# Kernel optimization log

Hardware: AMD Instinct MI355X
Metric: run time of the kernel (lower is better)

Reference implementation:

```python
import jax, jax.numpy as jnp
import numpy as np


def a_powers(A, t):
    # A: [K, n, n]; returns [t, K, n, n] = stack(I, A, A^2, ..., A^(t-1))
    K, n, _ = A.shape
    result = jnp.broadcast_to(jnp.eye(n, dtype=A.dtype), (1, K, n, n))
    lift = A
    while result.shape[0] < t:
        result = jnp.concatenate([result, result @ lift], axis=0)
        lift = lift @ lift
    return result[:t]


def fast_conv_real(a, b):
    # a: [len1, K, n, n], b: [batch, len2, K, n] -> conv(b, a): [batch, len1+len2-1, K, n]
    len1 = a.shape[0]
    len2 = b.shape[1]
    T = 2 ** int(np.ceil(np.log2(len1 + len2 - 1)))
    Af = jnp.fft.rfft(a, n=T, axis=0)
    Bf = jnp.fft.rfft(b, n=T, axis=1)
    Cf = jnp.einsum('blki,lkij->blkj', Bf, Af)
    c = jnp.fft.irfft(Cf, n=T, axis=1)
    return c[:, :len1 + len2 - 1]


def setup_inputs() -> dict:
    key = jax.random.key(0)
    k_u, k_x0, k_theta, k_B, k_C = jax.random.split(key, 5)
    batch, length = 8, 4096
    input_size, state_size, output_size = 256, 256, 256
    blk = 2
    K = state_size // blk  # 128
    u = jax.random.normal(k_u, (batch, length, input_size), dtype=jnp.float32)
    x0 = jax.random.normal(k_x0, (batch, K, blk), dtype=jnp.float32)
    # A initialized as K random 2x2 rotation blocks (as in __init__)
    theta = 2 * jnp.pi * jax.random.uniform(k_theta, (K,), dtype=jnp.float32)
    c, s = jnp.cos(theta), jnp.sin(theta)
    A = jnp.stack([jnp.stack([c, s], -1), jnp.stack([-s, c], -1)], -2)  # [K, 2, 2]
    B = jax.random.normal(k_B, (input_size, state_size), dtype=jnp.float32) / (state_size + input_size) ** 0.5
    C = jax.random.normal(k_C, (state_size, output_size), dtype=jnp.float32) / (state_size + output_size) ** 0.5
    return {"u": u, "x0": x0, "A": A, "B": B, "C": C}


def reference(u, x0, A, B, C):
    batch, length, _ = u.shape
    K, blk, _ = A.shape
    Aps = a_powers(A, length + 1)          # [length+1, K, blk, blk]
    uB = (u @ B).reshape(batch, length, K, blk)
    x = fast_conv_real(Aps[:-1], uB)[:, :length]  # [batch, length, K, blk]
    x = x + jnp.einsum('bki,lkij->blkj', x0, Aps[1:])
    new_state = x[:, -1]                    # [batch, K, blk]
    y = x.reshape(batch, length, K * blk) @ C
    return (y, new_state)
```

## Files before the change

kernel.cpp:

```cpp
#include <hip/hip_runtime.h>
#include <hip/hip_bf16.h>

typedef __bf16 bf16x2_t __attribute__((ext_vector_type(2)));
typedef __bf16 bf16x8_t __attribute__((ext_vector_type(8)));
typedef float f32x4 __attribute__((ext_vector_type(4)));

#define BATCH   8
#define LENGTH  4096
#define KHALF   128
#define MTOT    (BATCH*LENGTH)
#define NCHUNK  128
#define LC      32

#define SWZ(ch, row) ((ch) ^ ((row) & 7))

__global__ __launch_bounds__(256) void transpose_bc(
    const float* __restrict__ Bsrc, const float* __restrict__ Csrc,
    __bf16* __restrict__ BT, __bf16* __restrict__ CT) {
  const float* src = blockIdx.y ? Csrc : Bsrc;
  __bf16* dst      = blockIdx.y ? CT   : BT;
  int n  = blockIdx.x;
  int kk = threadIdx.x;
  dst[n * 256 + kk] = (__bf16)src[kk * 256 + n];
}

__global__ __launch_bounds__(256) void gemm1_fused(
    const float* __restrict__ u, const __bf16* __restrict__ BT,
    const float* __restrict__ Aarr,
    __bf16* __restrict__ uB, float2* __restrict__ P) {
  __shared__ __align__(16) __bf16 sA[64 * 256];

  const int tid  = threadIdx.x;
  const int lane = tid & 63;
  const int wave = tid >> 6;
  const int m_l  = lane & 15, quad = lane >> 4;
  const int m0   = blockIdx.x * 64;
  const int b    = m0 >> 12;
  const int t0   = m0 & 4095;

#pragma unroll
  for (int i = 0; i < 8; ++i) {
    int s   = tid + i * 256;
    int row = s >> 5, ch = s & 31;
    const float4* g = (const float4*)(u + (size_t)(m0 + row) * 256 + ch * 8);
    float4 a = g[0], c = g[1];
    bf16x8_t v;
    v[0]=(__bf16)a.x; v[1]=(__bf16)a.y; v[2]=(__bf16)a.z; v[3]=(__bf16)a.w;
    v[4]=(__bf16)c.x; v[5]=(__bf16)c.y; v[6]=(__bf16)c.z; v[7]=(__bf16)c.w;
    *(bf16x8_t*)&sA[row * 256 + SWZ(ch, row) * 8] = v;
  }
  __syncthreads();

  f32x4 acc[4][4];
#pragma unroll
  for (int mi = 0; mi < 4; ++mi)
#pragma unroll
    for (int ni = 0; ni < 4; ++ni)
#pragma unroll
      for (int r = 0; r < 4; ++r) acc[mi][ni][r] = 0.f;

#pragma unroll
  for (int kc8 = 0; kc8 < 8; ++kc8) {
    bf16x8_t af[4], bfr[4];
#pragma unroll
    for (int mi = 0; mi < 4; ++mi) {
      int row = mi * 16 + m_l;
      int c   = kc8 * 4 + quad;
      af[mi] = *(const bf16x8_t*)&sA[row * 256 + SWZ(c, row) * 8];
    }
#pragma unroll
    for (int ni = 0; ni < 4; ++ni) {
      int n = wave * 64 + ni * 16 + m_l;
      bfr[ni] = *(const bf16x8_t*)(BT + (size_t)n * 256 + kc8 * 32 + quad * 8);
    }
#pragma unroll
    for (int mi = 0; mi < 4; ++mi)
#pragma unroll
      for (int ni = 0; ni < 4; ++ni)
        acc[mi][ni] = __builtin_amdgcn_mfma_f32_16x16x32_bf16(af[mi], bfr[ni], acc[mi][ni], 0, 0, 0);
  }
  __syncthreads();

  __bf16* sT = sA;
#pragma unroll
  for (int mi = 0; mi < 4; ++mi)
#pragma unroll
    for (int ni = 0; ni < 4; ++ni)
#pragma unroll
      for (int r = 0; r < 4; ++r) {
        int row = mi * 16 + quad * 4 + r;
        int col = wave * 64 + ni * 16 + m_l;
        sT[row * 256 + SWZ(col >> 3, row) * 8 + (col & 7)] = (__bf16)acc[mi][ni][r];
      }
  __syncthreads();

#pragma unroll
  for (int i = 0; i < 8; ++i) {
    int s   = tid + i * 256;
    int row = s >> 5, ch = s & 31;
    *(bf16x8_t*)(uB + (size_t)(m0 + row) * 256 + ch * 8) =
        *(const bf16x8_t*)&sT[row * 256 + SWZ(ch, row) * 8];
  }

  {
    int k   = tid & 127;
    int chl = tid >> 7;
    float cc = Aarr[4 * k], sv = Aarr[4 * k + 1];
    float hr = 0.f, hi = 0.f;
#pragma unroll 8
    for (int j = 0; j < LC; ++j) {
      int row = chl * 32 + j;
      bf16x2_t v2 = *(const bf16x2_t*)&sT[row * 256 + SWZ(k >> 2, row) * 8 + ((2 * k) & 7)];
      float t = fmaf(hr, cc, fmaf(-hi, sv, (float)v2[0]));
      hi      = fmaf(hr, sv, fmaf( hi, cc, (float)v2[1]));
      hr = t;
    }
    int chg = (t0 >> 5) + chl;
    P[((size_t)b * NCHUNK + chg) * KHALF + k] = make_float2(hr, hi);
  }
}

__global__ __launch_bounds__(256) void scan_carry2(
    const float* __restrict__ Aarr, const float* __restrict__ x0,
    const float2* __restrict__ P, float2* __restrict__ H,
    float* __restrict__ state_out) {
  const int lane = threadIdx.x & 63;
  const int wv   = threadIdx.x >> 6;
  const int p    = blockIdx.x * 4 + wv;
  const int b    = p >> 7, k = p & 127;
  const float cc = Aarr[4 * k], sv = Aarr[4 * k + 1];

  float wr = cc, wi = sv;
#pragma unroll
  for (int i = 0; i < 5; ++i) { float nr = wr*wr - wi*wi; wi = 2.f*wr*wi; wr = nr; }
  float Wr[6], Wi[6];
  Wr[0] = wr*wr - wi*wi; Wi[0] = 2.f*wr*wi;
#pragma unroll
  for (int s = 1; s < 6; ++s) { Wr[s] = Wr[s-1]*Wr[s-1] - Wi[s-1]*Wi[s-1]; Wi[s] = 2.f*Wr[s-1]*Wi[s-1]; }

  float2 P0 = P[((size_t)b * NCHUNK + 2 * lane)     * KHALF + k];
  float2 P1 = P[((size_t)b * NCHUNK + 2 * lane + 1) * KHALF + k];
  float qr = fmaf(wr, P0.x, fmaf(-wi, P0.y, P1.x));
  float qi = fmaf(wr, P0.y, fmaf( wi, P0.x, P1.y));
  float Sr = qr, Si = qi;
#pragma unroll
  for (int s = 0; s < 6; ++s) {
    float tr = __shfl_up(Sr, 1 << s, 64);
    float ti = __shfl_up(Si, 1 << s, 64);
    if (lane >= (1 << s)) {
      float nSr = fmaf(Wr[s], tr, fmaf(-Wi[s], ti, Sr));
      float nSi = fmaf(Wr[s], ti, fmaf( Wi[s], tr, Si));
      Sr = nSr; Si = nSi;
    }
  }
  float Ar = __shfl_up(Sr, 1, 64), Ai = __shfl_up(Si, 1, 64);
  if (lane == 0) { Ar = 0.f; Ai = 0.f; }
  float pr = 1.f, pi = 0.f;
#pragma unroll
  for (int s = 0; s < 6; ++s)
    if ((lane >> s) & 1) { float nr = pr*Wr[s] - pi*Wi[s]; pi = pr*Wi[s] + pi*Wr[s]; pr = nr; }

  float x0r = x0[b * 256 + 2 * k], x0i = x0[b * 256 + 2 * k + 1];
  float H0r = fmaf(pr, x0r, fmaf(-pi, x0i, Ar));
  float H0i = fmaf(pr, x0i, fmaf( pi, x0r, Ai));
  H[((size_t)b * NCHUNK + 2 * lane) * KHALF + k] = make_float2(H0r, H0i);
  float H1r = fmaf(wr, H0r, fmaf(-wi, H0i, P0.x));
  float H1i = fmaf(wr, H0i, fmaf( wi, H0r, P0.y));
  H[((size_t)b * NCHUNK + 2 * lane + 1) * KHALF + k] = make_float2(H1r, H1i);
  if (lane == 63) {
    state_out[b * 256 + 2 * k]     = fmaf(wr, H1r, fmaf(-wi, H1i, P1.x));
    state_out[b * 256 + 2 * k + 1] = fmaf(wr, H1i, fmaf( wi, H1r, P1.y));
  }
}

__global__ __launch_bounds__(256) void gemm2_fused(
    const __bf16* __restrict__ uB, const float* __restrict__ Aarr,
    const float2* __restrict__ H, const __bf16* __restrict__ CT,
    float* __restrict__ Y) {
  __shared__ __align__(16) __bf16 sX[64 * 256];

  const int tid  = threadIdx.x;
  const int lane = tid & 63;
  const int wave = tid >> 6;
  const int m_l  = lane & 15, quad = lane >> 4;
  const int m0   = blockIdx.x * 64;
  const int b    = m0 >> 12;
  const int t0   = m0 & 4095;

#pragma unroll
  for (int i = 0; i < 8; ++i) {
    int s   = tid + i * 256;
    int row = s >> 5, ch = s & 31;
    *(bf16x8_t*)&sX[row * 256 + SWZ(ch, row) * 8] =
        *(const bf16x8_t*)(uB + (size_t)(m0 + row) * 256 + ch * 8);
  }
  __syncthreads();

  {
    int k   = tid & 127;
    int chl = tid >> 7;
    float cc = Aarr[4 * k], sv = Aarr[4 * k + 1];
    float2 h = H[((size_t)b * NCHUNK + (t0 >> 5) + chl) * KHALF + k];
    float hr = h.x, hi = h.y;
#pragma unroll 8
    for (int j = 0; j < LC; ++j) {
      int row = chl * 32 + j;
      int idx = row * 256 + SWZ(k >> 2, row) * 8 + ((2 * k) & 7);
      bf16x2_t v2 = *(const bf16x2_t*)&sX[idx];
      float t = fmaf(hr, cc, fmaf(-hi, sv, (float)v2[0]));
      hi      = fmaf(hr, sv, fmaf( hi, cc, (float)v2[1]));
      hr = t;
      bf16x2_t o; o[0] = (__bf16)hr; o[1] = (__bf16)hi;
      *(bf16x2_t*)&sX[idx] = o;
    }
  }
  __syncthreads();

  f32x4 acc[4][4];
#pragma unroll
  for (int mi = 0; mi < 4; ++mi)
#pragma unroll
    for (int ni = 0; ni < 4; ++ni)
#pragma unroll
      for (int r = 0; r < 4; ++r) acc[mi][ni][r] = 0.f;

#pragma unroll
  for (int kc8 = 0; kc8 < 8; ++kc8) {
    bf16x8_t af[4], bfr[4];
#pragma unroll
    for (int mi = 0; mi < 4; ++mi) {
      int row = mi * 16 + m_l;
      int c   = kc8 * 4 + quad;
      af[mi] = *(const bf16x8_t*)&sX[row * 256 + SWZ(c, row) * 8];
    }
#pragma unroll
    for (int ni = 0; ni < 4; ++ni) {
      int n = wave * 64 + ni * 16 + m_l;
      bfr[ni] = *(const bf16x8_t*)(CT + (size_t)n * 256 + kc8 * 32 + quad * 8);
    }
#pragma unroll
    for (int mi = 0; mi < 4; ++mi)
#pragma unroll
      for (int ni = 0; ni < 4; ++ni)
        acc[mi][ni] = __builtin_amdgcn_mfma_f32_16x16x32_bf16(af[mi], bfr[ni], acc[mi][ni], 0, 0, 0);
  }

#pragma unroll
  for (int mi = 0; mi < 4; ++mi)
#pragma unroll
    for (int ni = 0; ni < 4; ++ni)
#pragma unroll
      for (int r = 0; r < 4; ++r) {
        int row = m0 + mi * 16 + quad * 4 + r;
        int col = wave * 64 + ni * 16 + m_l;
        Y[(size_t)row * 256 + col] = acc[mi][ni][r];
      }
}

extern "C" void kernel_launch(void* const* d_in, const int* in_sizes, int n_in,
                              void* d_out, int out_size, void* d_ws, size_t ws_size,
                              hipStream_t stream) {
  const float* u  = (const float*)d_in[0];
  const float* x0 = (const float*)d_in[1];
  const float* A  = (const float*)d_in[2];
  const float* B  = (const float*)d_in[3];
  const float* C  = (const float*)d_in[4];

  float* y         = (float*)d_out;
  float* state_out = y + (size_t)MTOT * 256;

  char* ws = (char*)d_ws;
  __bf16* BT = (__bf16*)ws;  ws += 256 * 256 * 2;
  __bf16* CT = (__bf16*)ws;  ws += 256 * 256 * 2;
  __bf16* uB = (__bf16*)ws;  ws += (size_t)MTOT * 256 * 2;
  float2* P  = (float2*)ws;  ws += (size_t)BATCH * NCHUNK * KHALF * sizeof(float2);
  float2* H  = (float2*)ws;  ws += (size_t)BATCH * NCHUNK * KHALF * sizeof(float2);

  transpose_bc<<<dim3(256, 2), 256, 0, stream>>>(B, C, BT, CT);
  gemm1_fused<<<dim3(MTOT / 64), 256, 0, stream>>>(u, BT, A, uB, P);
  scan_carry2<<<dim3(256), 256, 0, stream>>>(A, x0, P, H, state_out);
  gemm2_fused<<<dim3(MTOT / 64), 256, 0, stream>>>(uB, A, H, CT, y);
}
```

Before: 119.4 us.

## Recompute u@B in output kernel instead of storing uB; fold carry scan inline

The first kernel no longer writes the bf16 uB intermediate and only emits per-chunk partial states P. The output kernel rereads u, recomputes the u@B GEMM, and computes each chunk's incoming carry by serially combining the preceding chunk partials from x0. This drops the separate scan kernel and one launch. It also removes the 16MB uB write and read. The cost is a second GEMM over u, a serial loop of up to 127 steps per thread, and a 32MB fp32 reread of u.

```diff
diff --git a/kernel.cpp b/kernel.cpp
--- a/kernel.cpp
+++ b/kernel.cpp
@@ -24,11 +24,10 @@
   dst[n * 256 + kk] = (__bf16)src[kk * 256 + n];
 }
 
-__global__ __launch_bounds__(256) void gemm1_fused(
+__global__ __launch_bounds__(256, 2) void gemm_p(
     const float* __restrict__ u, const __bf16* __restrict__ BT,
-    const float* __restrict__ Aarr,
-    __bf16* __restrict__ uB, float2* __restrict__ P) {
-  __shared__ __align__(16) __bf16 sA[64 * 256];
+    const float* __restrict__ Aarr, float2* __restrict__ P) {
+  __shared__ __align__(16) __bf16 sT[64 * 256];
 
   const int tid  = threadIdx.x;
   const int lane = tid & 63;
@@ -47,7 +46,7 @@
     bf16x8_t v;
     v[0]=(__bf16)a.x; v[1]=(__bf16)a.y; v[2]=(__bf16)a.z; v[3]=(__bf16)a.w;
     v[4]=(__bf16)c.x; v[5]=(__bf16)c.y; v[6]=(__bf16)c.z; v[7]=(__bf16)c.w;
-    *(bf16x8_t*)&sA[row * 256 + SWZ(ch, row) * 8] = v;
+    *(bf16x8_t*)&sT[row * 256 + SWZ(ch, row) * 8] = v;
   }
   __syncthreads();
 
@@ -66,7 +65,7 @@
     for (int mi = 0; mi < 4; ++mi) {
       int row = mi * 16 + m_l;
       int c   = kc8 * 4 + quad;
-      af[mi] = *(const bf16x8_t*)&sA[row * 256 + SWZ(c, row) * 8];
+      af[mi] = *(const bf16x8_t*)&sT[row * 256 + SWZ(c, row) * 8];
     }
 #pragma unroll
     for (int ni = 0; ni < 4; ++ni) {
@@ -81,7 +80,6 @@
   }
   __syncthreads();
 
-  __bf16* sT = sA;
 #pragma unroll
   for (int mi = 0; mi < 4; ++mi)
 #pragma unroll
@@ -93,14 +91,6 @@
         sT[row * 256 + SWZ(col >> 3, row) * 8 + (col & 7)] = (__bf16)acc[mi][ni][r];
       }
   __syncthreads();
-
-#pragma unroll
-  for (int i = 0; i < 8; ++i) {
-    int s   = tid + i * 256;
-    int row = s >> 5, ch = s & 31;
-    *(bf16x8_t*)(uB + (size_t)(m0 + row) * 256 + ch * 8) =
-        *(const bf16x8_t*)&sT[row * 256 + SWZ(ch, row) * 8];
-  }
 
   {
     int k   = tid & 127;
@@ -120,64 +110,12 @@
   }
 }
 
-__global__ __launch_bounds__(256) void scan_carry2(
-    const float* __restrict__ Aarr, const float* __restrict__ x0,
-    const float2* __restrict__ P, float2* __restrict__ H,
-    float* __restrict__ state_out) {
-  const int lane = threadIdx.x & 63;
-  const int wv   = threadIdx.x >> 6;
-  const int p    = blockIdx.x * 4 + wv;
-  const int b    = p >> 7, k = p & 127;
-  const float cc = Aarr[4 * k], sv = Aarr[4 * k + 1];
-
-  float wr = cc, wi = sv;
-#pragma unroll
-  for (int i = 0; i < 5; ++i) { float nr = wr*wr - wi*wi; wi = 2.f*wr*wi; wr = nr; }
-  float Wr[6], Wi[6];
-  Wr[0] = wr*wr - wi*wi; Wi[0] = 2.f*wr*wi;
-#pragma unroll
-  for (int s = 1; s < 6; ++s) { Wr[s] = Wr[s-1]*Wr[s-1] - Wi[s-1]*Wi[s-1]; Wi[s] = 2.f*Wr[s-1]*Wi[s-1]; }
-
-  float2 P0 = P[((size_t)b * NCHUNK + 2 * lane)     * KHALF + k];
-  float2 P1 = P[((size_t)b * NCHUNK + 2 * lane + 1) * KHALF + k];
-  float qr = fmaf(wr, P0.x, fmaf(-wi, P0.y, P1.x));
-  float qi = fmaf(wr, P0.y, fmaf( wi, P0.x, P1.y));
-  float Sr = qr, Si = qi;
-#pragma unroll
-  for (int s = 0; s < 6; ++s) {
-    float tr = __shfl_up(Sr, 1 << s, 64);
-    float ti = __shfl_up(Si, 1 << s, 64);
-    if (lane >= (1 << s)) {
-      float nSr = fmaf(Wr[s], tr, fmaf(-Wi[s], ti, Sr));
-      float nSi = fmaf(Wr[s], ti, fmaf( Wi[s], tr, Si));
-      Sr = nSr; Si = nSi;
-    }
-  }
-  float Ar = __shfl_up(Sr, 1, 64), Ai = __shfl_up(Si, 1, 64);
-  if (lane == 0) { Ar = 0.f; Ai = 0.f; }
-  float pr = 1.f, pi = 0.f;
-#pragma unroll
-  for (int s = 0; s < 6; ++s)
-    if ((lane >> s) & 1) { float nr = pr*Wr[s] - pi*Wi[s]; pi = pr*Wi[s] + pi*Wr[s]; pr = nr; }
-
-  float x0r = x0[b * 256 + 2 * k], x0i = x0[b * 256 + 2 * k + 1];
-  float H0r = fmaf(pr, x0r, fmaf(-pi, x0i, Ar));
-  float H0i = fmaf(pr, x0i, fmaf( pi, x0r, Ai));
-  H[((size_t)b * NCHUNK + 2 * lane) * KHALF + k] = make_float2(H0r, H0i);
-  float H1r = fmaf(wr, H0r, fmaf(-wi, H0i, P0.x));
-  float H1i = fmaf(wr, H0i, fmaf( wi, H0r, P0.y));
-  H[((size_t)b * NCHUNK + 2 * lane + 1) * KHALF + k] = make_float2(H1r, H1i);
-  if (lane == 63) {
-    state_out[b * 256 + 2 * k]     = fmaf(wr, H1r, fmaf(-wi, H1i, P1.x));
-    state_out[b * 256 + 2 * k + 1] = fmaf(wr, H1i, fmaf( wi, H1r, P1.y));
-  }
-}
-
-__global__ __launch_bounds__(256) void gemm2_fused(
-    const __bf16* __restrict__ uB, const float* __restrict__ Aarr,
-    const float2* __restrict__ H, const __bf16* __restrict__ CT,
-    float* __restrict__ Y) {
-  __shared__ __align__(16) __bf16 sX[64 * 256];
+__global__ __launch_bounds__(256, 2) void ssm_out(
+    const float* __restrict__ u, const __bf16* __restrict__ BT,
+    const __bf16* __restrict__ CT, const float* __restrict__ Aarr,
+    const float* __restrict__ x0, const float2* __restrict__ P,
+    float* __restrict__ state_out, float* __restrict__ Y) {
+  __shared__ __align__(16) __bf16 sT[64 * 256];
 
   const int tid  = threadIdx.x;
   const int lane = tid & 63;
@@ -191,32 +129,98 @@
   for (int i = 0; i < 8; ++i) {
     int s   = tid + i * 256;
     int row = s >> 5, ch = s & 31;
-    *(bf16x8_t*)&sX[row * 256 + SWZ(ch, row) * 8] =
-        *(const bf16x8_t*)(uB + (size_t)(m0 + row) * 256 + ch * 8);
-  }
-  __syncthreads();
-
+    const float4* g = (const float4*)(u + (size_t)(m0 + row) * 256 + ch * 8);
+    float4 a = g[0], c = g[1];
+    bf16x8_t v;
+    v[0]=(__bf16)a.x; v[1]=(__bf16)a.y; v[2]=(__bf16)a.z; v[3]=(__bf16)a.w;
+    v[4]=(__bf16)c.x; v[5]=(__bf16)c.y; v[6]=(__bf16)c.z; v[7]=(__bf16)c.w;
+    *(bf16x8_t*)&sT[row * 256 + SWZ(ch, row) * 8] = v;
+  }
+
+  const int k   = tid & 127;
+  const int chl = tid >> 7;
+  const int chg = (t0 >> 5) + chl;
+  const float cc = Aarr[4 * k], sv = Aarr[4 * k + 1];
+  float carry_r, carry_i;
   {
-    int k   = tid & 127;
-    int chl = tid >> 7;
-    float cc = Aarr[4 * k], sv = Aarr[4 * k + 1];
-    float2 h = H[((size_t)b * NCHUNK + (t0 >> 5) + chl) * KHALF + k];
-    float hr = h.x, hi = h.y;
+    float wr = cc, wi = sv;
+#pragma unroll
+    for (int i = 0; i < 5; ++i) { float nr = wr*wr - wi*wi; wi = 2.f*wr*wi; wr = nr; }
+    float hr = x0[b * 256 + 2 * k], hi = x0[b * 256 + 2 * k + 1];
+    const float2* pp = P + (size_t)b * NCHUNK * KHALF + k;
+#pragma unroll 4
+    for (int ch = 0; ch < chg; ++ch) {
+      float2 pv = pp[(size_t)ch * KHALF];
+      float t = fmaf(hr, wr, fmaf(-hi, wi, pv.x));
+      hi      = fmaf(hr, wi, fmaf( hi, wr, pv.y));
+      hr = t;
+    }
+    carry_r = hr; carry_i = hi;
+  }
+  __syncthreads();
+
+  f32x4 acc[4][4];
+#pragma unroll
+  for (int mi = 0; mi < 4; ++mi)
+#pragma unroll
+    for (int ni = 0; ni < 4; ++ni)
+#pragma unroll
+      for (int r = 0; r < 4; ++r) acc[mi][ni][r] = 0.f;
+
+#pragma unroll
+  for (int kc8 = 0; kc8 < 8; ++kc8) {
+    bf16x8_t af[4], bfr[4];
+#pragma unroll
+    for (int mi = 0; mi < 4; ++mi) {
+      int row = mi * 16 + m_l;
+      int c   = kc8 * 4 + quad;
+      af[mi] = *(const bf16x8_t*)&sT[row * 256 + SWZ(c, row) * 8];
+    }
+#pragma unroll
+    for (int ni = 0; ni < 4; ++ni) {
+      int n = wave * 64 + ni * 16 + m_l;
+      bfr[ni] = *(const bf16x8_t*)(BT + (size_t)n * 256 + kc8 * 32 + quad * 8);
+    }
+#pragma unroll
+    for (int mi = 0; mi < 4; ++mi)
+#pragma unroll
+      for (int ni = 0; ni < 4; ++ni)
+        acc[mi][ni] = __builtin_amdgcn_mfma_f32_16x16x32_bf16(af[mi], bfr[ni], acc[mi][ni], 0, 0, 0);
+  }
+  __syncthreads();
+
+#pragma unroll
+  for (int mi = 0; mi < 4; ++mi)
+#pragma unroll
+    for (int ni = 0; ni < 4; ++ni)
+#pragma unroll
+      for (int r = 0; r < 4; ++r) {
+        int row = mi * 16 + quad * 4 + r;
+        int col = wave * 64 + ni * 16 + m_l;
+        sT[row * 256 + SWZ(col >> 3, row) * 8 + (col & 7)] = (__bf16)acc[mi][ni][r];
+      }
+  __syncthreads();
+
+  {
+    float hr = carry_r, hi = carry_i;
 #pragma unroll 8
     for (int j = 0; j < LC; ++j) {
       int row = chl * 32 + j;
       int idx = row * 256 + SWZ(k >> 2, row) * 8 + ((2 * k) & 7);
-      bf16x2_t v2 = *(const bf16x2_t*)&sX[idx];
+      bf16x2_t v2 = *(const bf16x2_t*)&sT[idx];
       float t = fmaf(hr, cc, fmaf(-hi, sv, (float)v2[0]));
       hi      = fmaf(hr, sv, fmaf( hi, cc, (float)v2[1]));
       hr = t;
       bf16x2_t o; o[0] = (__bf16)hr; o[1] = (__bf16)hi;
-      *(bf16x2_t*)&sX[idx] = o;
-    }
-  }
-  __syncthreads();
-
-  f32x4 acc[4][4];
+      *(bf16x2_t*)&sT[idx] = o;
+    }
+    if (t0 == 4032 && chl == 1) {
+      state_out[b * 256 + 2 * k]     = hr;
+      state_out[b * 256 + 2 * k + 1] = hi;
+    }
+  }
+  __syncthreads();
+
 #pragma unroll
   for (int mi = 0; mi < 4; ++mi)
 #pragma unroll
@@ -231,7 +235,7 @@
     for (int mi = 0; mi < 4; ++mi) {
       int row = mi * 16 + m_l;
       int c   = kc8 * 4 + quad;
-      af[mi] = *(const bf16x8_t*)&sX[row * 256 + SWZ(c, row) * 8];
+      af[mi] = *(const bf16x8_t*)&sT[row * 256 + SWZ(c, row) * 8];
     }
 #pragma unroll
     for (int ni = 0; ni < 4; ++ni) {
@@ -272,12 +276,9 @@
   char* ws = (char*)d_ws;
   __bf16* BT = (__bf16*)ws;  ws += 256 * 256 * 2;
   __bf16* CT = (__bf16*)ws;  ws += 256 * 256 * 2;
-  __bf16* uB = (__bf16*)ws;  ws += (size_t)MTOT * 256 * 2;
   float2* P  = (float2*)ws;  ws += (size_t)BATCH * NCHUNK * KHALF * sizeof(float2);
-  float2* H  = (float2*)ws;  ws += (size_t)BATCH * NCHUNK * KHALF * sizeof(float2);
 
   transpose_bc<<<dim3(256, 2), 256, 0, stream>>>(B, C, BT, CT);
-  gemm1_fused<<<dim3(MTOT / 64), 256, 0, stream>>>(u, BT, A, uB, P);
-  scan_carry2<<<dim3(256), 256, 0, stream>>>(A, x0, P, H, state_out);
-  gemm2_fused<<<dim3(MTOT / 64), 256, 0, stream>>>(uB, A, H, CT, y);
-}
+  gemm_p<<<dim3(MTOT / 64), 256, 0, stream>>>(u, BT, A, P);
+  ssm_out<<<dim3(MTOT / 64), 256, 0, stream>>>(u, BT, CT, A, x0, P, state_out, y);
+}
```

Measured after the change: 129.2 us. +8.2%, slower.

## Fold chunk-carry scan into gemm2 by sequentially accumulating chunk summaries per block

Applied to the files above, without the earlier changes.

Removes the separate scan_carry2 kernel and the H buffer. Each gemm2 block now works out its own incoming carry by walking all earlier chunk summaries P for its batch with the 32-step power of A, starting from x0. The last block also writes the final state. This saves a kernel launch and a global round trip. The cost is redundant serial work that grows with chunk index, up to 127 dependent steps of loads and FMAs per thread before the GEMM. That tail lengthens the critical path for late blocks.

```diff
diff --git a/kernel.cpp b/kernel.cpp
--- a/kernel.cpp
+++ b/kernel.cpp
@@ -120,63 +120,11 @@
   }
 }
 
-__global__ __launch_bounds__(256) void scan_carry2(
-    const float* __restrict__ Aarr, const float* __restrict__ x0,
-    const float2* __restrict__ P, float2* __restrict__ H,
-    float* __restrict__ state_out) {
-  const int lane = threadIdx.x & 63;
-  const int wv   = threadIdx.x >> 6;
-  const int p    = blockIdx.x * 4 + wv;
-  const int b    = p >> 7, k = p & 127;
-  const float cc = Aarr[4 * k], sv = Aarr[4 * k + 1];
-
-  float wr = cc, wi = sv;
-#pragma unroll
-  for (int i = 0; i < 5; ++i) { float nr = wr*wr - wi*wi; wi = 2.f*wr*wi; wr = nr; }
-  float Wr[6], Wi[6];
-  Wr[0] = wr*wr - wi*wi; Wi[0] = 2.f*wr*wi;
-#pragma unroll
-  for (int s = 1; s < 6; ++s) { Wr[s] = Wr[s-1]*Wr[s-1] - Wi[s-1]*Wi[s-1]; Wi[s] = 2.f*Wr[s-1]*Wi[s-1]; }
-
-  float2 P0 = P[((size_t)b * NCHUNK + 2 * lane)     * KHALF + k];
-  float2 P1 = P[((size_t)b * NCHUNK + 2 * lane + 1) * KHALF + k];
-  float qr = fmaf(wr, P0.x, fmaf(-wi, P0.y, P1.x));
-  float qi = fmaf(wr, P0.y, fmaf( wi, P0.x, P1.y));
-  float Sr = qr, Si = qi;
-#pragma unroll
-  for (int s = 0; s < 6; ++s) {
-    float tr = __shfl_up(Sr, 1 << s, 64);
-    float ti = __shfl_up(Si, 1 << s, 64);
-    if (lane >= (1 << s)) {
-      float nSr = fmaf(Wr[s], tr, fmaf(-Wi[s], ti, Sr));
-      float nSi = fmaf(Wr[s], ti, fmaf( Wi[s], tr, Si));
-      Sr = nSr; Si = nSi;
-    }
-  }
-  float Ar = __shfl_up(Sr, 1, 64), Ai = __shfl_up(Si, 1, 64);
-  if (lane == 0) { Ar = 0.f; Ai = 0.f; }
-  float pr = 1.f, pi = 0.f;
-#pragma unroll
-  for (int s = 0; s < 6; ++s)
-    if ((lane >> s) & 1) { float nr = pr*Wr[s] - pi*Wi[s]; pi = pr*Wi[s] + pi*Wr[s]; pr = nr; }
-
-  float x0r = x0[b * 256 + 2 * k], x0i = x0[b * 256 + 2 * k + 1];
-  float H0r = fmaf(pr, x0r, fmaf(-pi, x0i, Ar));
-  float H0i = fmaf(pr, x0i, fmaf( pi, x0r, Ai));
-  H[((size_t)b * NCHUNK + 2 * lane) * KHALF + k] = make_float2(H0r, H0i);
-  float H1r = fmaf(wr, H0r, fmaf(-wi, H0i, P0.x));
-  float H1i = fmaf(wr, H0i, fmaf( wi, H0r, P0.y));
-  H[((size_t)b * NCHUNK + 2 * lane + 1) * KHALF + k] = make_float2(H1r, H1i);
-  if (lane == 63) {
-    state_out[b * 256 + 2 * k]     = fmaf(wr, H1r, fmaf(-wi, H1i, P1.x));
-    state_out[b * 256 + 2 * k + 1] = fmaf(wr, H1i, fmaf( wi, H1r, P1.y));
-  }
-}
-
 __global__ __launch_bounds__(256) void gemm2_fused(
     const __bf16* __restrict__ uB, const float* __restrict__ Aarr,
-    const float2* __restrict__ H, const __bf16* __restrict__ CT,
-    float* __restrict__ Y) {
+    const float* __restrict__ x0, const float2* __restrict__ P,
+    const __bf16* __restrict__ CT,
+    float* __restrict__ state_out, float* __restrict__ Y) {
   __shared__ __align__(16) __bf16 sX[64 * 256];
 
   const int tid  = threadIdx.x;
@@ -194,14 +142,31 @@
     *(bf16x8_t*)&sX[row * 256 + SWZ(ch, row) * 8] =
         *(const bf16x8_t*)(uB + (size_t)(m0 + row) * 256 + ch * 8);
   }
-  __syncthreads();
-
+
+  const int k   = tid & 127;
+  const int chl = tid >> 7;
+  const int chg = (t0 >> 5) + chl;
+  const float cc = Aarr[4 * k], sv = Aarr[4 * k + 1];
+  float carry_r, carry_i;
   {
-    int k   = tid & 127;
-    int chl = tid >> 7;
-    float cc = Aarr[4 * k], sv = Aarr[4 * k + 1];
-    float2 h = H[((size_t)b * NCHUNK + (t0 >> 5) + chl) * KHALF + k];
-    float hr = h.x, hi = h.y;
+    float wr = cc, wi = sv;
+#pragma unroll
+    for (int i = 0; i < 5; ++i) { float nr = wr*wr - wi*wi; wi = 2.f*wr*wi; wr = nr; }
+    float hr = x0[b * 256 + 2 * k], hi = x0[b * 256 + 2 * k + 1];
+    const float2* pp = P + (size_t)b * NCHUNK * KHALF + k;
+#pragma unroll 4
+    for (int ch = 0; ch < chg; ++ch) {
+      float2 pv = pp[(size_t)ch * KHALF];
+      float t = fmaf(hr, wr, fmaf(-hi, wi, pv.x));
+      hi      = fmaf(hr, wi, fmaf( hi, wr, pv.y));
+      hr = t;
+    }
+    carry_r = hr; carry_i = hi;
+  }
+  __syncthreads();
+
+  {
+    float hr = carry_r, hi = carry_i;
 #pragma unroll 8
     for (int j = 0; j < LC; ++j) {
       int row = chl * 32 + j;
@@ -213,6 +178,10 @@
       bf16x2_t o; o[0] = (__bf16)hr; o[1] = (__bf16)hi;
       *(bf16x2_t*)&sX[idx] = o;
     }
+    if (t0 == 4032 && chl == 1) {
+      state_out[b * 256 + 2 * k]     = hr;
+      state_out[b * 256 + 2 * k + 1] = hi;
+    }
   }
   __syncthreads();
 
@@ -274,10 +243,8 @@
   __bf16* CT = (__bf16*)ws;  ws += 256 * 256 * 2;
   __bf16* uB = (__bf16*)ws;  ws += (size_t)MTOT * 256 * 2;
   float2* P  = (float2*)ws;  ws += (size_t)BATCH * NCHUNK * KHALF * sizeof(float2);
-  float2* H  = (float2*)ws;  ws += (size_t)BATCH * NCHUNK * KHALF * sizeof(float2);
 
   transpose_bc<<<dim3(256, 2), 256, 0, stream>>>(B, C, BT, CT);
   gemm1_fused<<<dim3(MTOT / 64), 256, 0, stream>>>(u, BT, A, uB, P);
-  scan_carry2<<<dim3(256), 256, 0, stream>>>(A, x0, P, H, state_out);
-  gemm2_fused<<<dim3(MTOT / 64), 256, 0, stream>>>(uB, A, H, CT, y);
-}
+  gemm2_fused<<<dim3(MTOT / 64), 256, 0, stream>>>(uB, A, x0, P, CT, state_out, y);
+}
```

New measurement: 124.4 us. +4.2%, slower.
